# Optimization experiments

Hardware: AMD Instinct MI355X
Metric: run time of the kernel (lower is better)

Reference implementation:

```python
import jax, jax.numpy as jnp
import numpy as np

K = 32          # kernel_size == per-unit image side
GRID = 128      # SOM grid side (units)
H = K * GRID    # full SOM canvas side = 4096
EPS = 1e-8      # variance-weighting stabilizer


def setup_inputs() -> dict:
    key = jax.random.key(0)
    k1, k2, k3 = jax.random.split(key, 3)
    input_image = jax.random.uniform(k1, (K, K), dtype=jnp.float32)
    som_matrix = jax.random.uniform(k2, (H, H), dtype=jnp.float32)
    # variances kept strictly positive
    som_running_variances = jax.random.uniform(k3, (H, H), dtype=jnp.float32) + 0.1
    return {
        "input_image": input_image,
        "som_matrix": som_matrix,
        "som_running_variances": som_running_variances,
    }


def _box_sum(x, k):
    """k x k stride-1 VALID box-sum via integral image (avoids O(N*k^2) patches)."""
    s = jnp.cumsum(jnp.cumsum(x, axis=0), axis=1)
    s = jnp.pad(s, ((1, 0), (1, 0)))  # [H+1, H+1]
    return s[k:, k:] - s[:-k, k:] - s[k:, :-k] + s[:-k, :-k]  # [H-k+1, H-k+1]


def reference(input_image, som_matrix, som_running_variances):
    # build(): kernel = tile(input_image, som_grid)
    kernel = jnp.tile(input_image, (H // K, H // K))  # [H, H]
    # util.global_variance_distance: variance-weighted squared distance per pixel
    dist = (kernel - som_matrix) ** 2 / (som_running_variances + EPS)  # [H, H]
    # stride-1 k x k patch extraction + per-patch sum == box filter
    return _box_sum(dist, K)  # [H-K+1, H-K+1]
```

## Files before the change

kernel.cpp:

```cpp
#include <hip/hip_runtime.h>
#include <hip/hip_bf16.h>

#define HH 4096
#define KK 32
#define OH 4065
#define NB 225
#define BC 256
#define RCHUNK 64
#define GR 8

__global__ __launch_bounds__(256, 4) void som_fused(
    const float* __restrict__ img,
    const float* __restrict__ som,
    const float* __restrict__ var,
    float* __restrict__ out)
{
    __shared__ float simg[KK * KK];
    __shared__ float ldsv[2][GR][BC];
    __shared__ float ldsp[GR][BC];

    const int tid  = threadIdx.x;
    const int lane = tid & 63;
    const int wv   = tid >> 6;

    for (int i = tid; i < KK * KK; i += BC) simg[i] = img[i];

    const int c0   = blockIdx.x * NB;
    const int col  = c0 + tid;
    const int colc = col < HH ? col : HH - 1;
    const int jc   = col & (KK - 1);
    const int r0   = blockIdx.y * RCHUNK;

    __syncthreads();

    float ring[KK];
    float sum = 0.f;
#pragma unroll
    for (int t = 0; t < KK; ++t) {
        const int row = r0 + t;
        const float s  = som[row * HH + colc];
        const float v  = var[row * HH + colc];
        const float im = simg[((row & (KK - 1)) << 5) | jc];
        const float e  = im - s;
        const float d  = e * e * __builtin_amdgcn_rcpf(v + 1e-8f);
        ring[t] = d;
        sum += d;
    }

#pragma unroll
    for (int gi = 0; gi < RCHUNK / KK; ++gi) {
#pragma unroll
        for (int sg = 0; sg < KK / GR; ++sg) {
            const int buf = sg & 1;
#pragma unroll
            for (int k = 0; k < GR; ++k) {
                ldsv[buf][k][tid] = sum;
                int row = r0 + gi * KK + sg * GR + k + KK;
                row = row < HH ? row : HH - 1;
                const float s  = som[row * HH + colc];
                const float v  = var[row * HH + colc];
                const float im = simg[((row & (KK - 1)) << 5) | jc];
                const float e  = im - s;
                const float d  = e * e * __builtin_amdgcn_rcpf(v + 1e-8f);
                sum += d - ring[sg * GR + k];
                ring[sg * GR + k] = d;
            }
            __syncthreads();

#pragma unroll
            for (int rr = 0; rr < 2; ++rr) {
                const int k = 2 * wv + rr;
                float4 x = *(const float4*)&ldsv[buf][k][lane * 4];
                const float p0 = x.x;
                const float p1 = p0 + x.y;
                const float p2 = p1 + x.z;
                const float p3 = p2 + x.w;
                float sc = p3;
#pragma unroll
                for (int off = 1; off < 64; off <<= 1) {
                    const float t = __shfl_up(sc, off, 64);
                    sc += (lane >= off) ? t : 0.f;
                }
                const float excl = sc - p3;
                float4 o;
                o.x = p0 + excl; o.y = p1 + excl; o.z = p2 + excl; o.w = p3 + excl;
                *(float4*)&ldsp[k][lane * 4] = o;
            }
            __syncthreads();

            if (tid < NB && c0 + tid < OH) {
                const int c = tid;
                const float lo = (c > 0) ? ldsp[0][c - 1] : 0.f;
#pragma unroll
                for (int k = 0; k < GR; ++k) {
                    const int rout = r0 + gi * KK + sg * GR + k;
                    if (rout < OH) {
                        const float hi = ldsp[k][c + KK - 1];
                        const float l2 = (c > 0) ? ldsp[k][c - 1] : 0.f;
                        out[rout * OH + c0 + c] = hi - l2;
                    }
                }
                (void)lo;
            }
        }
    }
}

extern "C" void kernel_launch(void* const* d_in, const int* in_sizes, int n_in,
                              void* d_out, int out_size, void* d_ws, size_t ws_size,
                              hipStream_t stream) {
    (void)in_sizes; (void)n_in; (void)out_size; (void)d_ws; (void)ws_size;
    const float* img = (const float*)d_in[0];
    const float* som = (const float*)d_in[1];
    const float* var = (const float*)d_in[2];
    float* out = (float*)d_out;

    dim3 blk(BC);
    dim3 grd((OH + NB - 1) / NB,
             (OH + RCHUNK - 1) / RCHUNK);
    hipLaunchKernelGGL(som_fused, grd, blk, 0, stream, img, som, var, out);
}
```

Baseline: 206.0 us.

## Software-prefetch next row group into registers and use LDS-only barriers

Loads for the next group of rows are issued into a double-buffered register array before the current group is processed, so global memory latency overlaps the scan work. The __syncthreads calls are replaced with a barrier that waits only on LDS counters (vmcnt left outstanding), so in-flight global loads and stores are not drained at each barrier. The scan result is written back in place into ldsv, dropping the separate ldsp buffer and its LDS footprint. Register pressure rises from the prefetch arrays, which could hurt occupancy under launch_bounds(256,4).

```diff
diff --git a/kernel.cpp b/kernel.cpp
--- a/kernel.cpp
+++ b/kernel.cpp
@@ -8,8 +8,16 @@
 #define BC 256
 #define RCHUNK 64
 #define GR 8
+#define NSUB (RCHUNK / GR)
 
-__global__ __launch_bounds__(256, 4) void som_fused(
+__device__ __forceinline__ void barrier_lds_only() {
+    asm volatile("" ::: "memory");
+    __builtin_amdgcn_s_waitcnt(0xC07F);
+    __builtin_amdgcn_s_barrier();
+    asm volatile("" ::: "memory");
+}
+
+__global__ __launch_bounds__(BC, 4) void som_fused(
     const float* __restrict__ img,
     const float* __restrict__ som,
     const float* __restrict__ var,
@@ -17,90 +25,101 @@
 {
     __shared__ float simg[KK * KK];
     __shared__ float ldsv[2][GR][BC];
-    __shared__ float ldsp[GR][BC];
 
     const int tid  = threadIdx.x;
     const int lane = tid & 63;
     const int wv   = tid >> 6;
 
     for (int i = tid; i < KK * KK; i += BC) simg[i] = img[i];
+    __syncthreads();
 
     const int c0   = blockIdx.x * NB;
     const int col  = c0 + tid;
     const int colc = col < HH ? col : HH - 1;
     const int jc   = col & (KK - 1);
     const int r0   = blockIdx.y * RCHUNK;
+    const int maxoff = HH - 1 - r0;
 
-    __syncthreads();
+    const float* sp = som + (size_t)r0 * HH + colc;
+    const float* vp = var + (size_t)r0 * HH + colc;
 
     float ring[KK];
     float sum = 0.f;
 #pragma unroll
     for (int t = 0; t < KK; ++t) {
-        const int row = r0 + t;
-        const float s  = som[row * HH + colc];
-        const float v  = var[row * HH + colc];
-        const float im = simg[((row & (KK - 1)) << 5) | jc];
+        const float s  = sp[t * HH];
+        const float v  = vp[t * HH];
+        const float im = simg[(t << 5) | jc];
         const float e  = im - s;
         const float d  = e * e * __builtin_amdgcn_rcpf(v + 1e-8f);
         ring[t] = d;
         sum += d;
     }
 
+    float pf_s[2][GR], pf_v[2][GR];
 #pragma unroll
-    for (int gi = 0; gi < RCHUNK / KK; ++gi) {
+    for (int k = 0; k < GR; ++k) {
+        const int off = KK + k;
+        pf_s[0][k] = sp[off * HH];
+        pf_v[0][k] = vp[off * HH];
+    }
+
 #pragma unroll
-        for (int sg = 0; sg < KK / GR; ++sg) {
-            const int buf = sg & 1;
+    for (int sub = 0; sub < NSUB; ++sub) {
+        const int buf = sub & 1;
+
+#pragma unroll
+        for (int k = 0; k < GR; ++k) {
+            int off = KK + (sub + 1) * GR + k;
+            off = off <= maxoff ? off : maxoff;
+            pf_s[buf ^ 1][k] = sp[off * HH];
+            pf_v[buf ^ 1][k] = vp[off * HH];
+        }
+
+#pragma unroll
+        for (int k = 0; k < GR; ++k) {
+            ldsv[buf][k][tid] = sum;
+            const float s  = pf_s[buf][k];
+            const float v  = pf_v[buf][k];
+            const float im = simg[(((sub * GR + k) & (KK - 1)) << 5) | jc];
+            const float e  = im - s;
+            const float d  = e * e * __builtin_amdgcn_rcpf(v + 1e-8f);
+            const int ri   = (sub * GR + k) & (KK - 1);
+            sum += d - ring[ri];
+            ring[ri] = d;
+        }
+        barrier_lds_only();
+
+#pragma unroll
+        for (int rr = 0; rr < 2; ++rr) {
+            const int k = 2 * wv + rr;
+            float4 x = *(const float4*)&ldsv[buf][k][lane * 4];
+            const float p0 = x.x;
+            const float p1 = p0 + x.y;
+            const float p2 = p1 + x.z;
+            const float p3 = p2 + x.w;
+            float sc = p3;
+#pragma unroll
+            for (int off = 1; off < 64; off <<= 1) {
+                const float t = __shfl_up(sc, off, 64);
+                sc += (lane >= off) ? t : 0.f;
+            }
+            const float excl = sc - p3;
+            float4 o;
+            o.x = p0 + excl; o.y = p1 + excl; o.z = p2 + excl; o.w = p3 + excl;
+            *(float4*)&ldsv[buf][k][lane * 4] = o;
+        }
+        barrier_lds_only();
+
+        if (tid < NB && col < OH) {
 #pragma unroll
             for (int k = 0; k < GR; ++k) {
-                ldsv[buf][k][tid] = sum;
-                int row = r0 + gi * KK + sg * GR + k + KK;
-                row = row < HH ? row : HH - 1;
-                const float s  = som[row * HH + colc];
-                const float v  = var[row * HH + colc];
-                const float im = simg[((row & (KK - 1)) << 5) | jc];
-                const float e  = im - s;
-                const float d  = e * e * __builtin_amdgcn_rcpf(v + 1e-8f);
-                sum += d - ring[sg * GR + k];
-                ring[sg * GR + k] = d;
-            }
-            __syncthreads();
-
-#pragma unroll
-            for (int rr = 0; rr < 2; ++rr) {
-                const int k = 2 * wv + rr;
-                float4 x = *(const float4*)&ldsv[buf][k][lane * 4];
-                const float p0 = x.x;
-                const float p1 = p0 + x.y;
-                const float p2 = p1 + x.z;
-                const float p3 = p2 + x.w;
-                float sc = p3;
-#pragma unroll
-                for (int off = 1; off < 64; off <<= 1) {
-                    const float t = __shfl_up(sc, off, 64);
-                    sc += (lane >= off) ? t : 0.f;
+                const int rout = r0 + sub * GR + k;
+                if (rout < OH) {
+                    const float hi = ldsv[buf][k][tid + KK - 1];
+                    const float lo = (tid > 0) ? ldsv[buf][k][tid - 1] : 0.f;
+                    out[(size_t)rout * OH + col] = hi - lo;
                 }
-                const float excl = sc - p3;
-                float4 o;
-                o.x = p0 + excl; o.y = p1 + excl; o.z = p2 + excl; o.w = p3 + excl;
-                *(float4*)&ldsp[k][lane * 4] = o;
-            }
-            __syncthreads();
-
-            if (tid < NB && c0 + tid < OH) {
-                const int c = tid;
-                const float lo = (c > 0) ? ldsp[0][c - 1] : 0.f;
-#pragma unroll
-                for (int k = 0; k < GR; ++k) {
-                    const int rout = r0 + gi * KK + sg * GR + k;
-                    if (rout < OH) {
-                        const float hi = ldsp[k][c + KK - 1];
-                        const float l2 = (c > 0) ? ldsp[k][c - 1] : 0.f;
-                        out[rout * OH + c0 + c] = hi - l2;
-                    }
-                }
-                (void)lo;
             }
         }
     }
```

New measurement: 200.2 us. -2.8%, faster.
